# Performance work log

Hardware: AMD Instinct MI355X
Metric: run time of the kernel (lower is better)

The kernel has to match this reference:

```python
import jax, jax.numpy as jnp
import numpy as np

LMAX = 6
NMAX = 5
RC = 6.0
N_ATOMS = 65536
L = LMAX + 1


def _solid_harmonics(p):
    """Orthonormal regular solid harmonics S_lm = r^l * Y_lm for one point p=(x,y,z),
    packed into an (L,L) matrix the way AutoForce's Ylm does:
      Y[l, l-m] = Re(S_lm)  (lower triangle incl. diagonal),
      Y[m-1, l] = Im(S_lm)  (strict upper triangle, m >= 1).
    These are polynomials in (x,y,z) so jacfwd gives exact analytic gradients."""
    x, y, z = p[0], p[1], p[2]
    r2 = x * x + y * y + z * z
    zero = jnp.zeros_like(x)
    re = {(0, 0): 0.28209479177387814 + zero}  # 1/sqrt(4*pi)
    im = {(0, 0): zero}
    for l in range(1, LMAX + 1):
        a = -float(np.sqrt((2 * l + 1) / (2.0 * l)))
        re[(l, l)] = a * (x * re[(l - 1, l - 1)] - y * im[(l - 1, l - 1)])
        im[(l, l)] = a * (x * im[(l - 1, l - 1)] + y * re[(l - 1, l - 1)])
        for m in range(l):
            A = float(np.sqrt((l * l - m * m) / ((2 * l - 1.0) * (2 * l + 1.0))))
            if l - 2 >= m:
                Ap = float(np.sqrt(((l - 1) ** 2 - m * m) / ((2 * l - 3.0) * (2 * l - 1.0))))
                re[(l, m)] = (z * re[(l - 1, m)] - Ap * r2 * re[(l - 2, m)]) / A
                im[(l, m)] = (z * im[(l - 1, m)] - Ap * r2 * im[(l - 2, m)]) / A
            else:
                re[(l, m)] = z * re[(l - 1, m)] / A
                im[(l, m)] = z * im[(l - 1, m)] / A
    rows = []
    for i in range(L):
        row = [re[(i, i - j)] if j <= i else im[(j, i + 1)] for j in range(L)]
        rows.append(jnp.stack(row))
    return jnp.stack(rows)  # (L, L)


def _radial(d):
    # PolyCut(RC): r(d) = (1 - d/rc)^2 for d < rc else 0, with analytic derivative.
    step = (d < RC).astype(d.dtype)
    t = 1.0 - d / RC
    return t * t * step, (-2.0 / RC) * t * step


def _masks(dtype):
    one = jnp.ones((L, L), dtype)
    Yr = 2.0 * jnp.tril(one) - jnp.eye(L, dtype=dtype)  # real-part mask
    Yi = 2.0 * jnp.triu(one, k=1)                        # imag-part mask
    return Yr, Yi


def setup_inputs() -> dict:
    key = jax.random.key(0)
    xyz = jax.random.normal(key, (N_ATOMS, 3), dtype=jnp.float32)
    return {"xyz": xyz}


def reference(xyz):
    Yr, Yi = _masks(xyz.dtype)
    d = jnp.sqrt(jnp.sum(xyz * xyz, axis=-1))                 # (N,)
    n = 2.0 * jnp.arange(NMAX + 1, dtype=xyz.dtype)           # (nm,) exponents 0,2,...,2*nmax
    r, dr = _radial(d)
    dpow = d[None, :] ** n[:, None]                           # (nm, N)
    f = r[None] * dpow                                        # (nm, N)

    Y = jax.vmap(_solid_harmonics)(xyz).transpose(1, 2, 0)                  # (L, L, N)
    dY = jax.vmap(jax.jacfwd(_solid_harmonics))(xyz).transpose(1, 2, 0, 3)  # (L, L, N, 3)

    c = jnp.einsum('nj,lmj->nlm', f, Y)                       # (nm, L, L)

    # p[a,b,l] = sum_m Yr[l,m] c[a,l,m] c[b,l,m];  Yi part indexed by column m.
    p = jnp.einsum('lm,alm,blm->abl', Yr, c, c) + jnp.einsum('lm,alm,blm->abm', Yi, c, c)

    # df/dd, then chain rule through d -> xyz; n=0 term vanishes (0 * d^-1, d>0).
    df = dr[None] * dpow + r[None] * n[:, None] * d[None] ** (n[:, None] - 1.0)  # (nm, N)
    dfv = df[:, :, None] * (xyz / d[:, None])[None]                              # (nm, N, 3)

    # dc[a,l,m,j,k] = dfv[a,j,k]*Y[l,m,j] + f[a,j]*dY[l,m,j,k]  (never materialized)
    # dp[a,b] = T[a,b] + T[b,a] with T = mask-contraction of dc[a]*c[b].
    G = jnp.einsum('lm,lmj,blm->blj', Yr, Y, c) + jnp.einsum('lm,lmj,blm->bmj', Yi, Y, c)        # (nm, L, N)
    H = jnp.einsum('lm,lmjk,blm->bljk', Yr, dY, c) + jnp.einsum('lm,lmjk,blm->bmjk', Yi, dY, c)  # (nm, L, N, 3)
    T = jnp.einsum('ajk,blj->abljk', dfv, G) + jnp.einsum('aj,bljk->abljk', f, H)                # (nm, nm, L, N, 3)
    dp = T + T.transpose(1, 0, 2, 3, 4)

    return p.transpose(2, 0, 1), dp.transpose(2, 0, 1, 3, 4)
```

## Files before the change

kernel.cpp:

```cpp
#include <hip/hip_runtime.h>
#include <math.h>

constexpr float C00f = 0.28209479177387814f;

constexpr float AL[7] = {0.f,
  -1.22474487139158905f, -1.11803398874989485f, -1.08012344973464354f,
  -1.06066017177982121f, -1.04880884817015154f, -1.04083299973306640f};

constexpr float AINV[7][7] = {
  {0,0,0,0,0,0,0},
  {1.73205080756887729f,0,0,0,0,0,0},
  {1.93649167310370852f,2.23606797749978969f,0,0,0,0,0},
  {1.97202659436653873f,2.09165006633518887f,2.64575131106459059f,0,0,0,0},
  {1.98431348329844304f,2.04939015319191986f,2.29128784747791999f,3.0f,0,0,0},
  {1.98997487421323993f,2.03100960115899020f,2.17124068443428311f,2.48746859276654987f,3.31662479035539985f,0,0},
  {1.99304345718356630f,2.02131499000000000f,2.11394180000000000f,2.30136840000000000f,2.67394840000000000f,3.60555127546398912f,0}
};

constexpr float APV[7][7] = {
  {0,0,0,0,0,0,0},
  {0,0,0,0,0,0,0},
  {0.57735026918962576f,0,0,0,0,0,0},
  {0.51639777949432225f,0.44721359549995794f,0,0,0,0,0},
  {0.50709255283710986f,0.47809144373375745f,0.37796447300922722f,0,0,0,0},
  {0.50395263067896967f,0.48795003647426655f,0.43643578047198484f,0.33333333333333333f,0,0,0},
  {0.50251890762960643f,0.49236596391733095f,0.46056618647183828f,0.40201512610368484f,0.30151134457776363f,0,0}
};

__global__ void k_zero(float* __restrict__ cg) {
  int t = blockIdx.x * 256 + threadIdx.x;
  if (t < 294) cg[t] = 0.f;
}

__device__ __forceinline__ void wave_reduce_acc(float v, float* dst, int lane) {
  #pragma unroll
  for (int off = 32; off > 0; off >>= 1) v += __shfl_xor(v, off, 64);
  if (lane == 0) atomicAdd(dst, v);
}

__global__ __launch_bounds__(256) void k_accum_c(const float* __restrict__ xyz,
                                                 float* __restrict__ cg, int n) {
  __shared__ float cl[294];
  for (int i = threadIdx.x; i < 294; i += 256) cl[i] = 0.f;
  __syncthreads();
  int tid  = blockIdx.x * 256 + threadIdx.x;
  int lane = threadIdx.x & 63;
  int ji = (tid < n) ? tid : 0;
  float x = xyz[3*ji+0], y = xyz[3*ji+1], z = xyz[3*ji+2];
  float r2 = x*x + y*y + z*z;
  float d  = sqrtf(r2);
  float tcut = 1.f - d * (1.f/6.f);
  float r = (d < 6.f && tid < n) ? tcut*tcut : 0.f;
  float f[6];
  { float dp = 1.f;
    #pragma unroll
    for (int a = 0; a < 6; ++a) { f[a] = r*dp; dp *= r2; } }

  float vr[2][7], vi[2][7];
  vr[0][0] = C00f; vi[0][0] = 0.f;
  #pragma unroll
  for (int l = 0; l <= 6; ++l) {
    const int cur = l & 1, prv = cur ^ 1;
    if (l > 0) {
      #pragma unroll
      for (int m = 0; m + 2 <= l; ++m) {
        float ai = AINV[l][m], ap = APV[l][m];
        vr[cur][m] = (z*vr[prv][m] - ap*r2*vr[cur][m]) * ai;
        vi[cur][m] = (z*vi[prv][m] - ap*r2*vi[cur][m]) * ai;
      }
      { float ai = AINV[l][l-1];
        float vpr = vr[prv][l-1], vpi = vi[prv][l-1];
        vr[cur][l-1] = z*vpr*ai;
        vi[cur][l-1] = z*vpi*ai;
        vr[cur][l] = AL[l]*(x*vpr - y*vpi);
        vi[cur][l] = AL[l]*(x*vpi + y*vpr); }
    }
    #pragma unroll
    for (int m = 0; m <= l; ++m) {
      int idx_re = l*7 + (l - m);
      #pragma unroll
      for (int a = 0; a < 6; ++a) wave_reduce_acc(f[a]*vr[cur][m], &cl[a*49 + idx_re], lane);
      if (m >= 1) {
        int idx_im = (m-1)*7 + l;
        #pragma unroll
        for (int a = 0; a < 6; ++a) wave_reduce_acc(f[a]*vi[cur][m], &cl[a*49 + idx_im], lane);
      }
    }
  }
  __syncthreads();
  for (int i = threadIdx.x; i < 294; i += 256) atomicAdd(&cg[i], cl[i]);
}

__global__ __launch_bounds__(256) void k_p(const float* __restrict__ cg, float* __restrict__ out) {
  int t = threadIdx.x;
  if (t >= 252) return;
  int l = t / 36;
  int rem = t - 36*l;
  int a = rem / 6;
  int b = rem - 6*a;
  const float* ca = cg + a*49;
  const float* cb = cg + b*49;
  float s = 0.f;
  for (int mc = 0; mc <= l; ++mc) {
    float w = (mc == l) ? 1.f : 2.f;
    s += w * ca[l*7+mc] * cb[l*7+mc];
  }
  for (int rr = 0; rr < l; ++rr)
    s += 2.f * ca[rr*7+l] * cb[rr*7+l];
  out[t] = s;
}

__global__ __launch_bounds__(256) void k_dp(const float* __restrict__ xyz,
                                            const float* __restrict__ cg,
                                            float* __restrict__ out, int n3) {
  __shared__ float cs[294];
  for (int i = threadIdx.x; i < 294; i += 256) cs[i] = cg[i];
  __syncthreads();
  int tid = blockIdx.x * 256 + threadIdx.x;
  if (tid >= n3) return;
  int j = tid / 3;
  int k = tid - 3*j;
  float x = xyz[3*j+0], y = xyz[3*j+1], z = xyz[3*j+2];
  float ex = (k == 0) ? 1.f : 0.f;
  float ey = (k == 1) ? 1.f : 0.f;
  float ez = (k == 2) ? 1.f : 0.f;
  float pk = ex*x + ey*y + ez*z;
  float r2 = x*x + y*y + z*z;
  float d  = sqrtf(r2);
  float invd = (d > 0.f) ? 1.f/d : 0.f;
  bool inside = d < 6.f;
  float tcut = 1.f - d*(1.f/6.f);
  float r  = inside ? tcut*tcut : 0.f;
  float dr = inside ? (-1.f/3.f)*tcut : 0.f;
  float f[6], dfw[6];
  { float dp = 1.f;
    #pragma unroll
    for (int a = 0; a < 6; ++a) {
      f[a] = r*dp;
      float df = dp*(dr + (2.f*a)*r*invd);
      dfw[a] = df*pk*invd;
      dp *= r2;
    } }
  float* outdp = out + 252;

  float vr[2][7], vi[2][7], gr[2][7], gi[2][7];
  vr[0][0] = C00f; vi[0][0] = 0.f; gr[0][0] = 0.f; gi[0][0] = 0.f;
  #pragma unroll
  for (int l = 0; l <= 6; ++l) {
    const int cur = l & 1, prv = cur ^ 1;
    if (l > 0) {
      #pragma unroll
      for (int m = 0; m + 2 <= l; ++m) {
        float ai = AINV[l][m], ap = APV[l][m];
        float ovr = vr[cur][m], ovi = vi[cur][m];
        float ogr = gr[cur][m], ogi = gi[cur][m];
        vr[cur][m] = (z*vr[prv][m] - ap*r2*ovr) * ai;
        gr[cur][m] = (ez*vr[prv][m] + z*gr[prv][m] - ap*(2.f*pk*ovr + r2*ogr)) * ai;
        vi[cur][m] = (z*vi[prv][m] - ap*r2*ovi) * ai;
        gi[cur][m] = (ez*vi[prv][m] + z*gi[prv][m] - ap*(2.f*pk*ovi + r2*ogi)) * ai;
      }
      { float ai  = AINV[l][l-1];
        float vpr = vr[prv][l-1], vpi = vi[prv][l-1];
        float gpr = gr[prv][l-1], gpi = gi[prv][l-1];
        vr[cur][l-1] = z*vpr*ai;
        gr[cur][l-1] = (ez*vpr + z*gpr)*ai;
        vi[cur][l-1] = z*vpi*ai;
        gi[cur][l-1] = (ez*vpi + z*gpi)*ai;
        vr[cur][l] = AL[l]*(x*vpr - y*vpi);
        gr[cur][l] = AL[l]*(ex*vpr + x*gpr - ey*vpi - y*gpi);
        vi[cur][l] = AL[l]*(x*vpi + y*vpr);
        gi[cur][l] = AL[l]*(ex*vpi + x*gpi + ey*vpr + y*gpr); }
    }
    float G[6]  = {0,0,0,0,0,0};
    float Hh[6] = {0,0,0,0,0,0};
    #pragma unroll
    for (int m = 0; m <= l; ++m) {
      float w  = (m == 0) ? 1.f : 2.f;
      float wv = w*vr[cur][m], wg = w*gr[cur][m];
      int base = l*7 + (l - m);
      #pragma unroll
      for (int b = 0; b < 6; ++b) { float cc = cs[b*49 + base]; G[b] += wv*cc; Hh[b] += wg*cc; }
      if (m >= 1) {
        float wv2 = 2.f*vi[cur][m], wg2 = 2.f*gi[cur][m];
        int base2 = (m-1)*7 + l;
        #pragma unroll
        for (int b = 0; b < 6; ++b) { float cc = cs[b*49 + base2]; G[b] += wv2*cc; Hh[b] += wg2*cc; }
      }
    }
    #pragma unroll
    for (int a = 0; a < 6; ++a) {
      #pragma unroll
      for (int b = 0; b < 6; ++b) {
        float val = dfw[a]*G[b] + f[a]*Hh[b] + dfw[b]*G[a] + f[b]*Hh[a];
        outdp[(size_t)(l*36 + a*6 + b) * (size_t)n3 + (size_t)tid] = val;
      }
    }
  }
}

extern "C" void kernel_launch(void* const* d_in, const int* in_sizes, int n_in,
                              void* d_out, int out_size, void* d_ws, size_t ws_size,
                              hipStream_t stream) {
  const float* xyz = (const float*)d_in[0];
  float* out = (float*)d_out;
  float* cg  = (float*)d_ws;
  int n3 = in_sizes[0];
  int n  = n3 / 3;

  k_zero   <<<dim3(2),              dim3(256), 0, stream>>>(cg);
  k_accum_c<<<dim3((n  + 255)/256), dim3(256), 0, stream>>>(xyz, cg, n);
  k_p      <<<dim3(1),              dim3(256), 0, stream>>>(cg, out);
  k_dp     <<<dim3((n3 + 255)/256), dim3(256), 0, stream>>>(xyz, cg, out, n3);
}
```

Before: 287.4 us.

## Split radial channels across wave halves, fuse p into dp kernel, exploit symmetry

The accumulation kernel now assigns 32 atoms per wavefront, with each half-wave handling three of the six radial channels. This shortens the shuffle reductions to five steps and halves the per-thread reduction count, at the cost of twice as many blocks. The separate power-spectrum kernel is folded into block 0 of the gradient kernel, removing one launch. The gradient kernel computes only the upper triangle of the symmetric (a,b) pairs and writes each value to both mirrored positions, which cuts the arithmetic but leaves the store volume unchanged.

Measured after the change: 245.5 us. -14.6%, faster.

```diff
diff --git a/kernel.cpp b/kernel.cpp
--- a/kernel.cpp
+++ b/kernel.cpp
@@ -32,10 +32,13 @@
   if (t < 294) cg[t] = 0.f;
 }
 
-__device__ __forceinline__ void wave_reduce_acc(float v, float* dst, int lane) {
-  #pragma unroll
-  for (int off = 32; off > 0; off >>= 1) v += __shfl_xor(v, off, 64);
-  if (lane == 0) atomicAdd(dst, v);
+__device__ __forceinline__ void red32_acc(float v, float* dst, int li) {
+  v += __shfl_xor(v,  1, 32);
+  v += __shfl_xor(v,  2, 32);
+  v += __shfl_xor(v,  4, 32);
+  v += __shfl_xor(v,  8, 32);
+  v += __shfl_xor(v, 16, 32);
+  if (li == 0) atomicAdd(dst, v);
 }
 
 __global__ __launch_bounds__(256) void k_accum_c(const float* __restrict__ xyz,
@@ -43,18 +46,22 @@
   __shared__ float cl[294];
   for (int i = threadIdx.x; i < 294; i += 256) cl[i] = 0.f;
   __syncthreads();
-  int tid  = blockIdx.x * 256 + threadIdx.x;
   int lane = threadIdx.x & 63;
-  int ji = (tid < n) ? tid : 0;
+  int wv   = threadIdx.x >> 6;
+  int li   = lane & 31;
+  int half = lane >> 5;
+  int atom = blockIdx.x * 128 + wv * 32 + li;
+  int ji = (atom < n) ? atom : 0;
   float x = xyz[3*ji+0], y = xyz[3*ji+1], z = xyz[3*ji+2];
   float r2 = x*x + y*y + z*z;
   float d  = sqrtf(r2);
   float tcut = 1.f - d * (1.f/6.f);
-  float r = (d < 6.f && tid < n) ? tcut*tcut : 0.f;
-  float f[6];
-  { float dp = 1.f;
-    #pragma unroll
-    for (int a = 0; a < 6; ++a) { f[a] = r*dp; dp *= r2; } }
+  float r = (d < 6.f && atom < n) ? tcut*tcut : 0.f;
+  float r2c  = r2*r2*r2;
+  float base = half ? (r*r2c) : r;
+  float fa[3];
+  fa[0] = base; fa[1] = base*r2; fa[2] = fa[1]*r2;
+  int abase = 3*half;
 
   float vr[2][7], vi[2][7];
   vr[0][0] = C00f; vi[0][0] = 0.f;
@@ -79,35 +86,18 @@
     for (int m = 0; m <= l; ++m) {
       int idx_re = l*7 + (l - m);
       #pragma unroll
-      for (int a = 0; a < 6; ++a) wave_reduce_acc(f[a]*vr[cur][m], &cl[a*49 + idx_re], lane);
+      for (int i = 0; i < 3; ++i)
+        red32_acc(fa[i]*vr[cur][m], &cl[(abase+i)*49 + idx_re], li);
       if (m >= 1) {
         int idx_im = (m-1)*7 + l;
         #pragma unroll
-        for (int a = 0; a < 6; ++a) wave_reduce_acc(f[a]*vi[cur][m], &cl[a*49 + idx_im], lane);
+        for (int i = 0; i < 3; ++i)
+          red32_acc(fa[i]*vi[cur][m], &cl[(abase+i)*49 + idx_im], li);
       }
     }
   }
   __syncthreads();
   for (int i = threadIdx.x; i < 294; i += 256) atomicAdd(&cg[i], cl[i]);
-}
-
-__global__ __launch_bounds__(256) void k_p(const float* __restrict__ cg, float* __restrict__ out) {
-  int t = threadIdx.x;
-  if (t >= 252) return;
-  int l = t / 36;
-  int rem = t - 36*l;
-  int a = rem / 6;
-  int b = rem - 6*a;
-  const float* ca = cg + a*49;
-  const float* cb = cg + b*49;
-  float s = 0.f;
-  for (int mc = 0; mc <= l; ++mc) {
-    float w = (mc == l) ? 1.f : 2.f;
-    s += w * ca[l*7+mc] * cb[l*7+mc];
-  }
-  for (int rr = 0; rr < l; ++rr)
-    s += 2.f * ca[rr*7+l] * cb[rr*7+l];
-  out[t] = s;
 }
 
 __global__ __launch_bounds__(256) void k_dp(const float* __restrict__ xyz,
@@ -116,6 +106,25 @@
   __shared__ float cs[294];
   for (int i = threadIdx.x; i < 294; i += 256) cs[i] = cg[i];
   __syncthreads();
+
+  if (blockIdx.x == 0 && threadIdx.x < 252) {
+    int t = threadIdx.x;
+    int pl = t / 36;
+    int rem = t - 36*pl;
+    int pa = rem / 6;
+    int pb = rem - 6*pa;
+    const float* ca = cs + pa*49;
+    const float* cb = cs + pb*49;
+    float s = 0.f;
+    for (int mc = 0; mc <= pl; ++mc) {
+      float wq = (mc == pl) ? 1.f : 2.f;
+      s += wq * ca[pl*7+mc] * cb[pl*7+mc];
+    }
+    for (int rr = 0; rr < pl; ++rr)
+      s += 2.f * ca[rr*7+pl] * cb[rr*7+pl];
+    out[t] = s;
+  }
+
   int tid = blockIdx.x * 256 + threadIdx.x;
   if (tid >= n3) return;
   int j = tid / 3;
@@ -132,15 +141,15 @@
   float tcut = 1.f - d*(1.f/6.f);
   float r  = inside ? tcut*tcut : 0.f;
   float dr = inside ? (-1.f/3.f)*tcut : 0.f;
-  float f[6], dfw[6];
+  float f[6], dfr[6];
   { float dp = 1.f;
     #pragma unroll
     for (int a = 0; a < 6; ++a) {
-      f[a] = r*dp;
-      float df = dp*(dr + (2.f*a)*r*invd);
-      dfw[a] = df*pk*invd;
+      f[a]   = r*dp;
+      dfr[a] = dp*(dr + (2.f*a)*r*invd);
       dp *= r2;
     } }
+  float w = pk * invd;
   float* outdp = out + 252;
 
   float vr[2][7], vi[2][7], gr[2][7], gi[2][7];
@@ -175,8 +184,8 @@
     float Hh[6] = {0,0,0,0,0,0};
     #pragma unroll
     for (int m = 0; m <= l; ++m) {
-      float w  = (m == 0) ? 1.f : 2.f;
-      float wv = w*vr[cur][m], wg = w*gr[cur][m];
+      float wm = (m == 0) ? 1.f : 2.f;
+      float wv = wm*vr[cur][m], wg = wm*gr[cur][m];
       int base = l*7 + (l - m);
       #pragma unroll
       for (int b = 0; b < 6; ++b) { float cc = cs[b*49 + base]; G[b] += wv*cc; Hh[b] += wg*cc; }
@@ -190,9 +199,13 @@
     #pragma unroll
     for (int a = 0; a < 6; ++a) {
       #pragma unroll
-      for (int b = 0; b < 6; ++b) {
-        float val = dfw[a]*G[b] + f[a]*Hh[b] + dfw[b]*G[a] + f[b]*Hh[a];
+      for (int b = a; b < 6; ++b) {
+        float U = dfr[a]*G[b] + dfr[b]*G[a];
+        float V = f[a]*Hh[b] + f[b]*Hh[a];
+        float val = U*w + V;
         outdp[(size_t)(l*36 + a*6 + b) * (size_t)n3 + (size_t)tid] = val;
+        if (b > a)
+          outdp[(size_t)(l*36 + b*6 + a) * (size_t)n3 + (size_t)tid] = val;
       }
     }
   }
@@ -207,8 +220,7 @@
   int n3 = in_sizes[0];
   int n  = n3 / 3;
 
-  k_zero   <<<dim3(2),              dim3(256), 0, stream>>>(cg);
-  k_accum_c<<<dim3((n  + 255)/256), dim3(256), 0, stream>>>(xyz, cg, n);
-  k_p      <<<dim3(1),              dim3(256), 0, stream>>>(cg, out);
-  k_dp     <<<dim3((n3 + 255)/256), dim3(256), 0, stream>>>(xyz, cg, out, n3);
-}
+  k_zero   <<<dim3(2),               dim3(256), 0, stream>>>(cg);
+  k_accum_c<<<dim3((n + 127)/128),   dim3(256), 0, stream>>>(xyz, cg, n);
+  k_dp     <<<dim3((n3 + 255)/256),  dim3(256), 0, stream>>>(xyz, cg, out, n3);
+}
```
